# Performance work log

Measured on AMD Instinct MI355X. Metric: run time of the kernel, lower is better.

## Reference

```python
import jax, jax.numpy as jnp
import numpy as np

N_NODES = 50000
N_EDGES = 800000
IN_DIM = 128
HID = 64
N_GRAPHS = 256


def gcn_conv(x, W, b, src, dst, num_nodes):
    """PyG GCNConv: add self-loops, sym norm D^-1/2 (A+I) D^-1/2, linear, bias."""
    h = x @ W  # [N, out]
    loop = jnp.arange(num_nodes)
    s = jnp.concatenate([src, loop])
    d = jnp.concatenate([dst, loop])
    ones = jnp.ones(d.shape, h.dtype)
    deg = jax.ops.segment_sum(ones, d, num_segments=num_nodes)
    dinv = jnp.where(deg > 0, jax.lax.rsqrt(deg), 0.0)
    norm = dinv[s] * dinv[d]  # [E+N]
    msg = h[s] * norm[:, None]  # gather + scale (memory bound)
    out = jax.ops.segment_sum(msg, d, num_segments=num_nodes)  # scatter-add
    return out + b


def setup_inputs() -> dict:
    key = jax.random.key(0)
    ks = jax.random.split(key, 8)
    x = jax.random.normal(ks[0], (N_NODES, IN_DIM), dtype=jnp.float32)
    edge_index = jax.random.randint(ks[1], (2, N_EDGES), 0, N_NODES, dtype=jnp.int64)
    batch = jnp.sort(jax.random.randint(ks[2], (N_NODES,), 0, N_GRAPHS, dtype=jnp.int64))
    W1 = jax.random.normal(ks[3], (IN_DIM, HID), dtype=jnp.float32) / np.sqrt(IN_DIM)
    b1 = jnp.zeros((HID,), jnp.float32)
    W2 = jax.random.normal(ks[4], (HID, HID), dtype=jnp.float32) / np.sqrt(HID)
    b2 = jnp.zeros((HID,), jnp.float32)
    Wl = jax.random.normal(ks[5], (HID, 1), dtype=jnp.float32) / np.sqrt(HID)
    bl = jnp.zeros((1,), jnp.float32)
    return {"x": x, "W1": W1, "b1": b1, "W2": W2, "b2": b2,
            "Wl": Wl, "bl": bl, "edge_index": edge_index, "batch": batch}


def reference(x, W1, b1, W2, b2, Wl, bl, edge_index, batch):
    n = x.shape[0]
    src, dst = edge_index[0], edge_index[1]
    h = jax.nn.relu(gcn_conv(x, W1, b1, src, dst, n))
    # dropout is identity in eval mode
    h = jax.nn.relu(gcn_conv(h, W2, b2, src, dst, n))
    ones = jnp.ones((n,), h.dtype)
    counts = jax.ops.segment_sum(ones, batch, num_segments=N_GRAPHS)
    pooled = jax.ops.segment_sum(h, batch, num_segments=N_GRAPHS)
    pooled = pooled / jnp.maximum(counts, 1.0)[:, None]  # global_mean_pool
    return (pooled @ Wl + bl).reshape(-1)  # [N_GRAPHS]
```

## Files before the change

### kernel.cpp

```cpp
#include <hip/hip_runtime.h>
#include <hip/hip_fp16.h>
#include <math.h>

__global__ void zero32(int* __restrict__ p, int n) {
    int i = blockIdx.x * blockDim.x + threadIdx.x;
    if (i < n) p[i] = 0;
}

__global__ void hist_rank(const int* __restrict__ dst, int* __restrict__ cnt,
                          unsigned short* __restrict__ rank, int E) {
    int e = blockIdx.x * blockDim.x + threadIdx.x;
    if (e < E) rank[e] = (unsigned short)atomicAdd(&cnt[dst[e]], 1);
}

__global__ __launch_bounds__(256) void scan1_dinv(const int* __restrict__ cnt,
                                                  int* __restrict__ excl,
                                                  int* __restrict__ sums,
                                                  float* __restrict__ dinv, int n) {
    int i = blockIdx.x * 256 + threadIdx.x;
    int v = (i < n) ? cnt[i] : 0;
    if (i < n) dinv[i] = rsqrtf((float)(v + 1));
    int lane = threadIdx.x & 63;
    int w = threadIdx.x >> 6;
    int s = v;
#pragma unroll
    for (int off = 1; off < 64; off <<= 1) {
        int t = __shfl_up(s, off, 64);
        if (lane >= off) s += t;
    }
    __shared__ int wsum[4];
    if (lane == 63) wsum[w] = s;
    __syncthreads();
    int woff = 0;
#pragma unroll
    for (int k = 0; k < 3; ++k) if (k < w) woff += wsum[k];
    int incl = s + woff;
    if (i < n) excl[i] = incl - v;
    if (threadIdx.x == 255) sums[blockIdx.x] = incl;
}

__global__ __launch_bounds__(256) void scan2(int* __restrict__ sums, int nb) {
    int t = threadIdx.x;
    int v = (t < nb) ? sums[t] : 0;
    int lane = t & 63;
    int w = t >> 6;
    int s = v;
#pragma unroll
    for (int off = 1; off < 64; off <<= 1) {
        int u = __shfl_up(s, off, 64);
        if (lane >= off) s += u;
    }
    __shared__ int wsum[4];
    if (lane == 63) wsum[w] = s;
    __syncthreads();
    int woff = 0;
#pragma unroll
    for (int k = 0; k < 3; ++k) if (k < w) woff += wsum[k];
    int incl = s + woff;
    if (t < nb) sums[t] = incl - v;
}

__global__ __launch_bounds__(256) void scan3(const int* __restrict__ excl,
                                             const int* __restrict__ sums,
                                             int* __restrict__ rowptr, int n, int E) {
    int i = blockIdx.x * 256 + threadIdx.x;
    if (i < n) rowptr[i] = excl[i] + sums[i >> 8];
    if (i == n) rowptr[n] = E;
}

__global__ void fill_place(const int* __restrict__ src, const int* __restrict__ dst,
                           const unsigned short* __restrict__ rank,
                           const int* __restrict__ rowptr,
                           unsigned short* __restrict__ col, int E, int n) {
    const int g    = blockIdx.x & 7;
    const int nblk = gridDim.x >> 3;
    const int bid  = blockIdx.x >> 3;
    const int lo = (int)(((long)g * n) >> 3);
    const int hi = (int)(((long)(g + 1) * n) >> 3);
    for (long e = (long)bid * blockDim.x + threadIdx.x; e < E;
         e += (long)nblk * blockDim.x) {
        int d = dst[e];
        if (d < lo || d >= hi) continue;
        col[rowptr[d] + rank[e]] = (unsigned short)src[e];
    }
}

#define RL(x, k) __int_as_float(__builtin_amdgcn_readlane(__float_as_int(x), (k)))

template <int K>
__global__ __launch_bounds__(256) void gemm_bcast_scaled(const float* __restrict__ X,
                                                         const float* __restrict__ W,
                                                         const float* __restrict__ dinv,
                                                         __half* __restrict__ Y, int n) {
    const int lane = threadIdx.x & 63;
    const long wid = (((long)blockIdx.x * blockDim.x) + threadIdx.x) >> 6;
    const long nw  = ((long)gridDim.x * blockDim.x) >> 6;

    float wr[K];
#pragma unroll
    for (int k = 0; k < K; ++k) wr[k] = W[k * 64 + lane];
#pragma unroll
    for (int k = 0; k < K; ++k) asm volatile("" : "+v"(wr[k]));

    long r0 = wid;
    if (r0 >= n) return;
    float xa0 = X[r0 * K + lane];
    float xb0 = 0.f;
    if constexpr (K > 64) xb0 = X[r0 * K + 64 + lane];
    float dv0 = dinv[r0];

    long r1 = r0 + nw;
    bool h1 = r1 < n;
    long rc1 = h1 ? r1 : r0;
    float xa1 = X[rc1 * K + lane];
    float xb1 = 0.f;
    if constexpr (K > 64) xb1 = X[rc1 * K + 64 + lane];
    float dv1 = dinv[rc1];

    while (true) {
        long r2 = r1 + nw;
        bool h2 = h1 && (r2 < n);
        long rc2 = h2 ? r2 : r0;
        float xa2 = X[rc2 * K + lane];
        float xb2 = 0.f;
        if constexpr (K > 64) xb2 = X[rc2 * K + 64 + lane];
        float dv2 = dinv[rc2];

        float a0 = 0.f, a1 = 0.f, a2 = 0.f, a3 = 0.f;
#pragma unroll
        for (int k = 0; k < 64; k += 4) {
            a0 = fmaf(RL(xa0, k + 0), wr[k + 0], a0);
            a1 = fmaf(RL(xa0, k + 1), wr[k + 1], a1);
            a2 = fmaf(RL(xa0, k + 2), wr[k + 2], a2);
            a3 = fmaf(RL(xa0, k + 3), wr[k + 3], a3);
        }
        if constexpr (K > 64) {
#pragma unroll
            for (int k = 0; k < 64; k += 4) {
                a0 = fmaf(RL(xb0, k + 0), wr[64 + k + 0], a0);
                a1 = fmaf(RL(xb0, k + 1), wr[64 + k + 1], a1);
                a2 = fmaf(RL(xb0, k + 2), wr[64 + k + 2], a2);
                a3 = fmaf(RL(xb0, k + 3), wr[64 + k + 3], a3);
            }
        }
        Y[r0 * 64 + lane] = __float2half(dv0 * ((a0 + a1) + (a2 + a3)));
        if (!h1) break;
        r0 = r1; xa0 = xa1; xb0 = xb1; dv0 = dv1;
        r1 = r2; h1 = h2; xa1 = xa2; xb1 = xb2; dv1 = dv2;
    }
}

#define HG(idx) __half2float(Hp[(long)(idx) * 64 + j])
__device__ __forceinline__ void agg2(const __half* __restrict__ Hp,
                                     const int* __restrict__ rowptr,
                                     const unsigned short* __restrict__ col,
                                     long vA, long vB, int j, bool hasB,
                                     float& sumA, float& sumB) {
    float a0 = HG(vA), a1 = 0.f, a2 = 0.f, a3 = 0.f;
    float b0 = 0.f, b1 = 0.f, b2 = 0.f, b3 = 0.f;
    int pA = rowptr[vA], pA1 = rowptr[vA + 1];
    int pB = 0, pB1 = 0;
    if (hasB) { b0 = HG(vB); pB = rowptr[vB]; pB1 = rowptr[vB + 1]; }
    if ((pA & 1) && pA < pA1) { a1 += HG(col[pA]); ++pA; }
    if ((pB & 1) && pB < pB1) { b1 += HG(col[pB]); ++pB; }
    unsigned int cA01 = *(const unsigned int*)(col + pA);
    unsigned int cA23 = *(const unsigned int*)(col + pA + 2);
    unsigned int cB01 = *(const unsigned int*)(col + pB);
    unsigned int cB23 = *(const unsigned int*)(col + pB + 2);
    while (pA + 4 <= pA1 && pB + 4 <= pB1) {
        unsigned int nA01 = *(const unsigned int*)(col + pA + 4);
        unsigned int nA23 = *(const unsigned int*)(col + pA + 6);
        unsigned int nB01 = *(const unsigned int*)(col + pB + 4);
        unsigned int nB23 = *(const unsigned int*)(col + pB + 6);
        float hA0 = HG(cA01 & 0xFFFFu);
        float hA1 = HG(cA01 >> 16);
        float hA2 = HG(cA23 & 0xFFFFu);
        float hA3 = HG(cA23 >> 16);
        float hB0 = HG(cB01 & 0xFFFFu);
        float hB1 = HG(cB01 >> 16);
        float hB2 = HG(cB23 & 0xFFFFu);
        float hB3 = HG(cB23 >> 16);
        a0 += hA0; a1 += hA1; a2 += hA2; a3 += hA3;
        b0 += hB0; b1 += hB1; b2 += hB2; b3 += hB3;
        cA01 = nA01; cA23 = nA23; cB01 = nB01; cB23 = nB23;
        pA += 4; pB += 4;
    }
    for (; pA + 4 <= pA1; pA += 4) {
        float h0 = HG(cA01 & 0xFFFFu);
        float h1 = HG(cA01 >> 16);
        float h2 = HG(cA23 & 0xFFFFu);
        float h3 = HG(cA23 >> 16);
        a0 += h0; a1 += h1; a2 += h2; a3 += h3;
        cA01 = *(const unsigned int*)(col + pA + 4);
        cA23 = *(const unsigned int*)(col + pA + 6);
    }
    for (; pA < pA1; ++pA) a1 += HG(col[pA]);
    for (; pB + 4 <= pB1; pB += 4) {
        float h0 = HG(cB01 & 0xFFFFu);
        float h1 = HG(cB01 >> 16);
        float h2 = HG(cB23 & 0xFFFFu);
        float h3 = HG(cB23 >> 16);
        b0 += h0; b1 += h1; b2 += h2; b3 += h3;
        cB01 = *(const unsigned int*)(col + pB + 4);
        cB23 = *(const unsigned int*)(col + pB + 6);
    }
    for (; pB < pB1; ++pB) b1 += HG(col[pB]);
    sumA = (a0 + a1) + (a2 + a3);
    sumB = (b0 + b1) + (b2 + b3);
}

__global__ __launch_bounds__(256) void agg_gemm64(const __half* __restrict__ Hp,
                                                  const int* __restrict__ rowptr,
                                                  const unsigned short* __restrict__ col,
                                                  const float* __restrict__ dinv,
                                                  const float* __restrict__ bias,
                                                  const float* __restrict__ W2,
                                                  __half* __restrict__ out, int n) {
    const int j = threadIdx.x & 63;
    const long wid = (((long)blockIdx.x * blockDim.x) + threadIdx.x) >> 6;
    const long NW  = ((long)gridDim.x * blockDim.x) >> 6;
    const float bj = bias[j];
    for (long vA = wid; vA < n; vA += 2 * NW) {
        long vB = vA + NW;
        bool hasB = vB < n;
        float sA, sB;
        agg2(Hp, rowptr, col, vA, vB, j, hasB, sA, sB);
        float diA = dinv[vA];
        float diB = hasB ? dinv[vB] : 0.f;
        float gA = fmaxf(diA * sA + bj, 0.f);
        float gB = fmaxf(diB * sB + bj, 0.f);
        float a0 = 0.f, a1 = 0.f, a2 = 0.f, a3 = 0.f;
        float b0 = 0.f, b1 = 0.f, b2 = 0.f, b3 = 0.f;
#pragma unroll
        for (int k = 0; k < 64; k += 4) {
            float w0 = W2[(k + 0) * 64 + j];
            float w1 = W2[(k + 1) * 64 + j];
            float w2 = W2[(k + 2) * 64 + j];
            float w3 = W2[(k + 3) * 64 + j];
            a0 = fmaf(RL(gA, k + 0), w0, a0);
            b0 = fmaf(RL(gB, k + 0), w0, b0);
            a1 = fmaf(RL(gA, k + 1), w1, a1);
            b1 = fmaf(RL(gB, k + 1), w1, b1);
            a2 = fmaf(RL(gA, k + 2), w2, a2);
            b2 = fmaf(RL(gB, k + 2), w2, b2);
            a3 = fmaf(RL(gA, k + 3), w3, a3);
            b3 = fmaf(RL(gB, k + 3), w3, b3);
        }
        out[vA * 64 + j] = __float2half(diA * ((a0 + a1) + (a2 + a3)));
        if (hasB) out[vB * 64 + j] = __float2half(diB * ((b0 + b1) + (b2 + b3)));
    }
}

__global__ __launch_bounds__(256) void agg_pool(const __half* __restrict__ Hp,
                                                const int* __restrict__ rowptr,
                                                const unsigned short* __restrict__ col,
                                                const float* __restrict__ dinv,
                                                const float* __restrict__ bias,
                                                const float* __restrict__ Wl,
                                                const int* __restrict__ batch,
                                                float* __restrict__ part,
                                                float* __restrict__ partc, int n) {
    __shared__ float lp[256];
    __shared__ float lc[256];
    lp[threadIdx.x] = 0.f;
    lc[threadIdx.x] = 0.f;
    __syncthreads();
    const int j  = threadIdx.x & 63;
    const int wv = threadIdx.x >> 6;
    const float bj  = bias[j];
    const float wlj = Wl[j];
    const long wid = (long)blockIdx.x * 4 + wv;
    const long NW  = (long)gridDim.x * 4;
    for (long vA = wid; vA < n; vA += 2 * NW) {
        long vB = vA + NW;
        bool hasB = vB < n;
        float sA, sB;
        agg2(Hp, rowptr, col, vA, vB, j, hasB, sA, sB);
        float diA = dinv[vA];
        float diB = hasB ? dinv[vB] : 0.f;
        float valA = fmaxf(diA * sA + bj, 0.f) * wlj;
        float valB = fmaxf(diB * sB + bj, 0.f) * wlj;
#pragma unroll
        for (int off = 32; off > 0; off >>= 1) {
            valA += __shfl_down(valA, off, 64);
            valB += __shfl_down(valB, off, 64);
        }
        if (j == 0) {
            atomicAdd(&lp[batch[vA]], valA);
            atomicAdd(&lc[batch[vA]], 1.0f);
            if (hasB) {
                atomicAdd(&lp[batch[vB]], valB);
                atomicAdd(&lc[batch[vB]], 1.0f);
            }
        }
    }
    __syncthreads();
    long o = (long)blockIdx.x * 256 + threadIdx.x;
    part[o]  = lp[threadIdx.x];
    partc[o] = lc[threadIdx.x];
}

__global__ __launch_bounds__(256) void pool_final(const float* __restrict__ part,
                                                  const float* __restrict__ partc,
                                                  const float* __restrict__ bl,
                                                  float* __restrict__ out, int nblk) {
    int g = blockIdx.x;
    int t = threadIdx.x;
    float s = 0.f, c = 0.f;
    for (int b = t; b < nblk; b += 256) {
        s += part[(long)b * 256 + g];
        c += partc[(long)b * 256 + g];
    }
    __shared__ float sp[256];
    __shared__ float sc[256];
    sp[t] = s;
    sc[t] = c;
    __syncthreads();
    for (int off = 128; off > 0; off >>= 1) {
        if (t < off) { sp[t] += sp[t + off]; sc[t] += sc[t + off]; }
        __syncthreads();
    }
    if (t == 0) out[g] = sp[0] / fmaxf(sc[0], 1.0f) + bl[0];
}

extern "C" void kernel_launch(void* const* d_in, const int* in_sizes, int n_in,
                              void* d_out, int out_size, void* d_ws, size_t ws_size,
                              hipStream_t stream) {
    const float* x  = (const float*)d_in[0];
    const float* W1 = (const float*)d_in[1];
    const float* b1 = (const float*)d_in[2];
    const float* W2 = (const float*)d_in[3];
    const float* b2 = (const float*)d_in[4];
    const float* Wl = (const float*)d_in[5];
    const float* bl = (const float*)d_in[6];
    const int* edge_index = (const int*)d_in[7];
    const int* batch      = (const int*)d_in[8];

    const int n = in_sizes[0] / 128;
    const int E = in_sizes[7] / 2;
    const int G = out_size;
    const int* src = edge_index;
    const int* dst = edge_index + E;

    char* ws = (char*)d_ws;
    size_t off = 0;
    auto alloc = [&](size_t bytes) { void* p = ws + off; off = (off + bytes + 255) & ~(size_t)255; return p; };
    int*            cntv   = (int*)           alloc((size_t)n * 4);
    float*          dinv   = (float*)         alloc((size_t)n * 4);
    int*            rowptr = (int*)           alloc((size_t)(n + 1) * 4);
    int*            excl   = (int*)           alloc((size_t)n * 4);
    int*            sums   = (int*)           alloc((size_t)256 * 4);
    unsigned short* rank   = (unsigned short*)alloc((size_t)E * 2);
    unsigned short* col    = (unsigned short*)alloc((size_t)E * 2 + 64);
    __half*         bufA   = (__half*)        alloc((size_t)n * 64 * 2);
    __half*         bufB   = (__half*)        alloc((size_t)n * 64 * 2);
    const int PBLK = 2048;
    float*          part   = (float*)         alloc((size_t)PBLK * 256 * 4);
    float*          partc  = (float*)         alloc((size_t)PBLK * 256 * 4);

    const int T = 256;
    const int nchunks = (n + 255) / 256;
    zero32<<<(n + T - 1) / T, T, 0, stream>>>(cntv, n);
    hist_rank<<<(E + T - 1) / T, T, 0, stream>>>(dst, cntv, rank, E);
    scan1_dinv<<<nchunks, T, 0, stream>>>(cntv, excl, sums, dinv, n);
    scan2<<<1, T, 0, stream>>>(sums, nchunks);
    scan3<<<(n + 1 + T - 1) / T, T, 0, stream>>>(excl, sums, rowptr, n, E);
    fill_place<<<1024, T, 0, stream>>>(src, dst, rank, rowptr, col, E, n);

    gemm_bcast_scaled<128><<<768, T, 0, stream>>>(x, W1, dinv, bufA, n);
    agg_gemm64<<<2048, T, 0, stream>>>(bufA, rowptr, col, dinv, b1, W2, bufB, n);
    agg_pool<<<PBLK, T, 0, stream>>>(bufB, rowptr, col, dinv, b2, Wl, batch, part, partc, n);
    pool_final<<<G, T, 0, stream>>>(part, partc, bl, (float*)d_out, PBLK);
}
```

Measured before the change: 209.0 us.

## Split layer-2 aggregation from its GEMM into separate kernels

The fused aggregate-plus-GEMM kernel is split in two. A lighter kernel, agg_relu16, only aggregates neighbours, applies bias and ReLU, and writes fp16 to a new buffer. The existing broadcast GEMM kernel, now templated to accept fp16 input, then does the W2 multiply. The aim is to remove the per-node W2 reloads and readlane work, and the register pressure they cause, from the latency-bound gather loop. In exchange it adds a kernel launch and an extra fp16 N×64 write and read round trip.

Result: faster. 171.8 us (-17.8%).

```diff
diff --git a/kernel.cpp b/kernel.cpp
--- a/kernel.cpp
+++ b/kernel.cpp
@@ -87,8 +87,11 @@
 
 #define RL(x, k) __int_as_float(__builtin_amdgcn_readlane(__float_as_int(x), (k)))
 
-template <int K>
-__global__ __launch_bounds__(256) void gemm_bcast_scaled(const float* __restrict__ X,
+__device__ __forceinline__ float ldf(const float* p, long i) { return p[i]; }
+__device__ __forceinline__ float ldf(const __half* p, long i) { return __half2float(p[i]); }
+
+template <int K, typename XT>
+__global__ __launch_bounds__(256) void gemm_bcast_scaled(const XT* __restrict__ X,
                                                          const float* __restrict__ W,
                                                          const float* __restrict__ dinv,
                                                          __half* __restrict__ Y, int n) {
@@ -104,26 +107,26 @@
 
     long r0 = wid;
     if (r0 >= n) return;
-    float xa0 = X[r0 * K + lane];
+    float xa0 = ldf(X, r0 * K + lane);
     float xb0 = 0.f;
-    if constexpr (K > 64) xb0 = X[r0 * K + 64 + lane];
+    if constexpr (K > 64) xb0 = ldf(X, r0 * K + 64 + lane);
     float dv0 = dinv[r0];
 
     long r1 = r0 + nw;
     bool h1 = r1 < n;
     long rc1 = h1 ? r1 : r0;
-    float xa1 = X[rc1 * K + lane];
+    float xa1 = ldf(X, rc1 * K + lane);
     float xb1 = 0.f;
-    if constexpr (K > 64) xb1 = X[rc1 * K + 64 + lane];
+    if constexpr (K > 64) xb1 = ldf(X, rc1 * K + 64 + lane);
     float dv1 = dinv[rc1];
 
     while (true) {
         long r2 = r1 + nw;
         bool h2 = h1 && (r2 < n);
         long rc2 = h2 ? r2 : r0;
-        float xa2 = X[rc2 * K + lane];
+        float xa2 = ldf(X, rc2 * K + lane);
         float xb2 = 0.f;
-        if constexpr (K > 64) xb2 = X[rc2 * K + 64 + lane];
+        if constexpr (K > 64) xb2 = ldf(X, rc2 * K + 64 + lane);
         float dv2 = dinv[rc2];
 
         float a0 = 0.f, a1 = 0.f, a2 = 0.f, a3 = 0.f;
@@ -209,12 +212,11 @@
     sumB = (b0 + b1) + (b2 + b3);
 }
 
-__global__ __launch_bounds__(256) void agg_gemm64(const __half* __restrict__ Hp,
+__global__ __launch_bounds__(256) void agg_relu16(const __half* __restrict__ Hp,
                                                   const int* __restrict__ rowptr,
                                                   const unsigned short* __restrict__ col,
                                                   const float* __restrict__ dinv,
                                                   const float* __restrict__ bias,
-                                                  const float* __restrict__ W2,
                                                   __half* __restrict__ out, int n) {
     const int j = threadIdx.x & 63;
     const long wid = (((long)blockIdx.x * blockDim.x) + threadIdx.x) >> 6;
@@ -227,27 +229,8 @@
         agg2(Hp, rowptr, col, vA, vB, j, hasB, sA, sB);
         float diA = dinv[vA];
         float diB = hasB ? dinv[vB] : 0.f;
-        float gA = fmaxf(diA * sA + bj, 0.f);
-        float gB = fmaxf(diB * sB + bj, 0.f);
-        float a0 = 0.f, a1 = 0.f, a2 = 0.f, a3 = 0.f;
-        float b0 = 0.f, b1 = 0.f, b2 = 0.f, b3 = 0.f;
-#pragma unroll
-        for (int k = 0; k < 64; k += 4) {
-            float w0 = W2[(k + 0) * 64 + j];
-            float w1 = W2[(k + 1) * 64 + j];
-            float w2 = W2[(k + 2) * 64 + j];
-            float w3 = W2[(k + 3) * 64 + j];
-            a0 = fmaf(RL(gA, k + 0), w0, a0);
-            b0 = fmaf(RL(gB, k + 0), w0, b0);
-            a1 = fmaf(RL(gA, k + 1), w1, a1);
-            b1 = fmaf(RL(gB, k + 1), w1, b1);
-            a2 = fmaf(RL(gA, k + 2), w2, a2);
-            b2 = fmaf(RL(gB, k + 2), w2, b2);
-            a3 = fmaf(RL(gA, k + 3), w3, a3);
-            b3 = fmaf(RL(gB, k + 3), w3, b3);
-        }
-        out[vA * 64 + j] = __float2half(diA * ((a0 + a1) + (a2 + a3)));
-        if (hasB) out[vB * 64 + j] = __float2half(diB * ((b0 + b1) + (b2 + b3)));
+        out[vA * 64 + j] = __float2half(fmaxf(diA * sA + bj, 0.f));
+        if (hasB) out[vB * 64 + j] = __float2half(fmaxf(diB * sB + bj, 0.f));
     }
 }
 
@@ -353,6 +336,7 @@
     unsigned short* rank   = (unsigned short*)alloc((size_t)E * 2);
     unsigned short* col    = (unsigned short*)alloc((size_t)E * 2 + 64);
     __half*         bufA   = (__half*)        alloc((size_t)n * 64 * 2);
+    __half*         bufC   = (__half*)        alloc((size_t)n * 64 * 2);
     __half*         bufB   = (__half*)        alloc((size_t)n * 64 * 2);
     const int PBLK = 2048;
     float*          part   = (float*)         alloc((size_t)PBLK * 256 * 4);
@@ -368,7 +352,8 @@
     fill_place<<<1024, T, 0, stream>>>(src, dst, rank, rowptr, col, E, n);
 
     gemm_bcast_scaled<128><<<768, T, 0, stream>>>(x, W1, dinv, bufA, n);
-    agg_gemm64<<<2048, T, 0, stream>>>(bufA, rowptr, col, dinv, b1, W2, bufB, n);
+    agg_relu16<<<2048, T, 0, stream>>>(bufA, rowptr, col, dinv, b1, bufC, n);
+    gemm_bcast_scaled<64><<<768, T, 0, stream>>>(bufC, W2, dinv, bufB, n);
     agg_pool<<<PBLK, T, 0, stream>>>(bufB, rowptr, col, dinv, b2, Wl, batch, part, partc, n);
     pool_final<<<G, T, 0, stream>>>(part, partc, bl, (float*)d_out, PBLK);
 }
```
